# Kernel tuning notes

Measured on AMD Instinct MI355X. Metric: run time of the kernel, lower is better.

## Reference

```python
import jax, jax.numpy as jnp
import numpy as np

EPS = 1e-5

def wn(v, g):
    # weight_norm dim=0: each output row scaled to norm g
    return v * (g / jnp.linalg.norm(v, axis=1))[:, None]

def layernorm(h):
    mu = jnp.mean(h, axis=-1, keepdims=True)
    var = jnp.mean(jnp.square(h - mu), axis=-1, keepdims=True)
    return (h - mu) / jnp.sqrt(var + EPS)

def setup_inputs() -> dict:
    key = jax.random.key(0)
    ks = jax.random.split(key, 12)
    N, G = 200000, 256
    node_dim, cond_dim, out_dim = 256, 256, 512
    H = out_dim // 2  # 256
    s = lambda d: 1.0 / np.sqrt(d)
    return {
        "x": jax.random.normal(ks[0], (N, node_dim), jnp.float32),
        "cond": jax.random.normal(ks[1], (G, cond_dim), jnp.float32),
        "batch_ids": jax.random.randint(ks[2], (N,), 0, G, jnp.int32),
        # FiLM cond projection: Linear(cond_dim, 2H) weight-normed, with bias
        "v_cond": jax.random.normal(ks[3], (2 * H, cond_dim), jnp.float32) * s(cond_dim),
        "g_cond": jnp.ones((2 * H,), jnp.float32),
        "b_cond": jnp.zeros((2 * H,), jnp.float32),
        # FiLM main linear: Linear(node_dim, H) weight-normed, no bias
        "v1": jax.random.normal(ks[4], (H, node_dim), jnp.float32) * s(node_dim),
        "g1": jnp.ones((H,), jnp.float32),
        # head MLP: Linear(H,H)+ReLU+Linear(H,out_dim), both weight-normed, with bias
        "v2": jax.random.normal(ks[5], (H, H), jnp.float32) * s(H),
        "g2": jnp.ones((H,), jnp.float32),
        "b2": jnp.zeros((H,), jnp.float32),
        "v3": jax.random.normal(ks[6], (out_dim, H), jnp.float32) * s(H),
        "g3": jnp.ones((out_dim,), jnp.float32),
        "b3": jnp.zeros((out_dim,), jnp.float32),
    }

def reference(x, cond, batch_ids, v_cond, g_cond, b_cond, v1, g1, v2, g2, b2, v3, g3, b3):
    H = v1.shape[0]
    # per-graph FiLM params
    gb = cond @ wn(v_cond, g_cond).T + b_cond          # [G, 2H]
    gamma = gb[:, :H] + 1.0                            # [G, H]
    beta = gb[:, H:]                                   # [G, H]
    # node path: linear (no bias) + layernorm (no affine)
    h = layernorm(x @ wn(v1, g1).T)                    # [N, H]
    # gather per-graph FiLM to nodes, modulate, relu
    h = jax.nn.relu(h * gamma[batch_ids] + beta[batch_ids])
    # head MLP
    h = jax.nn.relu(h @ wn(v2, g2).T + b2)             # [N, H]
    logits = h @ wn(v3, g3).T + b3                     # [N, out_dim]
    return logits
```

## Files before the change

kernel.cpp:

```cpp
#include <hip/hip_runtime.h>

typedef __bf16 bf16x8 __attribute__((ext_vector_type(8)));
typedef float f32x16 __attribute__((ext_vector_type(16)));

#define K_DIM 256

__global__ void wn_kernel(const float* __restrict__ v, const float* __restrict__ gv,
                          __bf16* __restrict__ dstb, float* __restrict__ dstf) {
  const int r = blockIdx.x;
  const int l = threadIdx.x;
  const float* vr = v + (size_t)r * K_DIM;
  float4 p = *reinterpret_cast<const float4*>(vr + l * 4);
  float ss = p.x * p.x + p.y * p.y + p.z * p.z + p.w * p.w;
#pragma unroll
  for (int m = 1; m <= 32; m <<= 1) ss += __shfl_xor(ss, m, 64);
  const float sc = gv[r] * rsqrtf(ss);
  const float a0 = p.x * sc, a1 = p.y * sc, a2 = p.z * sc, a3 = p.w * sc;
  if (dstf != nullptr) {
    float4 o; o.x = a0; o.y = a1; o.z = a2; o.w = a3;
    *reinterpret_cast<float4*>(dstf + (size_t)r * K_DIM + l * 4) = o;
  }
  if (dstb != nullptr) {
    const int rows = gridDim.x;
    __bf16* d = dstb + ((size_t)(l >> 1) * rows + r) * 8 + (l & 1) * 4;
    d[0] = (__bf16)a0; d[1] = (__bf16)a1; d[2] = (__bf16)a2; d[3] = (__bf16)a3;
  }
}

__global__ void gb_kernel(const float* __restrict__ cond, const float* __restrict__ wncf,
                          const float* __restrict__ bc, float* __restrict__ gbuf) {
  const int gidx = blockIdx.x;
  const int t = threadIdx.x;
  __shared__ float c[256];
  c[t] = cond[(size_t)gidx * 256 + t];
  __syncthreads();
#pragma unroll
  for (int h = 0; h < 2; ++h) {
    const int o = (h << 8) + t;
    const float* wr = wncf + (size_t)o * 256;
    float s = 0.0f;
#pragma unroll 8
    for (int k = 0; k < 256; k += 4) {
      const float4 w4 = *reinterpret_cast<const float4*>(wr + k);
      s += c[k] * w4.x + c[k + 1] * w4.y + c[k + 2] * w4.z + c[k + 3] * w4.w;
    }
    gbuf[(size_t)gidx * 512 + o] = s + bc[o] + (h == 0 ? 1.0f : 0.0f);
  }
}

__global__ __launch_bounds__(128, 2) void fused_kernel(
    const float* __restrict__ x, const int* __restrict__ bids,
    const __bf16* __restrict__ W1t, const __bf16* __restrict__ W2t,
    const __bf16* __restrict__ W3t, const float* __restrict__ gbuf,
    const float* __restrict__ b2, const float* __restrict__ b3,
    float* __restrict__ out, const int n) {
  __shared__ __bf16 Abuf[32 * 64 * 8];
  __shared__ __bf16 Wbuf[4 * 256 * 8];

  const int t = threadIdx.x;
  const int lane = t & 63;
  const int wave = t >> 6;
  const int nlo = lane & 31;
  const int g = lane >> 5;
  const int mbase = wave << 5;
  const int R = blockIdx.x << 6;

  f32x16 zero;
#pragma unroll
  for (int e = 0; e < 16; ++e) zero[e] = 0.0f;

  f32x16 acc[8];

  auto stage_w = [&](const __bf16* wsrc, int kt, int outr, int outbase) {
#pragma unroll
    for (int it = 0; it < 8; ++it) {
      const int cid = (((wave << 3) + it) << 6) + lane;
      const int kc = cid >> 8;
      const int outl = cid & 255;
      const __bf16* gp = wsrc + ((size_t)((kt * 4 + kc) * outr + outbase + outl) << 3);
      __builtin_amdgcn_global_load_lds(
          (__attribute__((address_space(1))) void*)gp,
          (__attribute__((address_space(3))) void*)(&Wbuf[((wave << 3) + it) << 9]),
          16, 0, 0);
    }
  };

#pragma unroll
  for (int nt = 0; nt < 8; ++nt) acc[nt] = zero;
  {
    int row = R + mbase + nlo;
    if (row >= n) row = n - 1;
    const float* xrow = x + (size_t)row * K_DIM;
    for (int kt = 0; kt < 8; ++kt) {
      __syncthreads();
      stage_w(W1t, kt, 256, 0);
      __syncthreads();
#pragma unroll
      for (int ks = 0; ks < 2; ++ks) {
        const int k0 = kt * 32 + ks * 16 + g * 8;
        const float4 p = *reinterpret_cast<const float4*>(xrow + k0);
        const float4 q = *reinterpret_cast<const float4*>(xrow + k0 + 4);
        bf16x8 a;
        a[0] = (__bf16)p.x; a[1] = (__bf16)p.y; a[2] = (__bf16)p.z; a[3] = (__bf16)p.w;
        a[4] = (__bf16)q.x; a[5] = (__bf16)q.y; a[6] = (__bf16)q.z; a[7] = (__bf16)q.w;
#pragma unroll
        for (int nt = 0; nt < 8; ++nt) {
          const bf16x8 b = *reinterpret_cast<const bf16x8*>(
              &Wbuf[((((ks << 1) + g) << 8) + (nt << 5) + nlo) << 3]);
          acc[nt] = __builtin_amdgcn_mfma_f32_32x32x16_bf16(a, b, acc[nt], 0, 0, 0);
        }
      }
    }
  }

  {
    float mu[16], rs[16];
#pragma unroll
    for (int reg = 0; reg < 16; ++reg) {
      float s = 0.0f, q = 0.0f;
#pragma unroll
      for (int nt = 0; nt < 8; ++nt) {
        const float v = acc[nt][reg];
        s += v; q += v * v;
      }
#pragma unroll
      for (int m = 1; m <= 16; m <<= 1) {
        s += __shfl_xor(s, m, 64);
        q += __shfl_xor(q, m, 64);
      }
      const float mean = s * (1.0f / 256.0f);
      const float var = q * (1.0f / 256.0f) - mean * mean;
      mu[reg] = mean;
      rs[reg] = rsqrtf(var + 1e-5f);
    }
#pragma unroll
    for (int reg = 0; reg < 16; ++reg) {
      const int rl = (reg & 3) + ((reg >> 2) << 3) + (g << 2);
      int rglob = R + mbase + rl;
      if (rglob >= n) rglob = n - 1;
      const int bid = bids[rglob];
      const float* grow = gbuf + ((size_t)bid << 9);
#pragma unroll
      for (int nt = 0; nt < 8; ++nt) {
        const int col = (nt << 5) + nlo;
        float v = (acc[nt][reg] - mu[reg]) * rs[reg];
        v = v * grow[col] + grow[256 + col];
        v = v > 0.0f ? v : 0.0f;
        Abuf[((((col >> 3) << 6) + mbase + rl) << 3) + (col & 7)] = (__bf16)v;
      }
    }
  }

#pragma unroll
  for (int nt = 0; nt < 8; ++nt) acc[nt] = zero;
  for (int kt = 0; kt < 8; ++kt) {
    __syncthreads();
    stage_w(W2t, kt, 256, 0);
    __syncthreads();
#pragma unroll
    for (int ks = 0; ks < 2; ++ks) {
      const int kc = kt * 4 + ks * 2 + g;
      const bf16x8 a = *reinterpret_cast<const bf16x8*>(
          &Abuf[((kc << 6) + mbase + nlo) << 3]);
#pragma unroll
      for (int nt = 0; nt < 8; ++nt) {
        const bf16x8 b = *reinterpret_cast<const bf16x8*>(
            &Wbuf[((((ks << 1) + g) << 8) + (nt << 5) + nlo) << 3]);
        acc[nt] = __builtin_amdgcn_mfma_f32_32x32x16_bf16(a, b, acc[nt], 0, 0, 0);
      }
    }
  }
  {
    float b2v[8];
#pragma unroll
    for (int nt = 0; nt < 8; ++nt) b2v[nt] = b2[(nt << 5) + nlo];
#pragma unroll
    for (int reg = 0; reg < 16; ++reg) {
      const int rl = (reg & 3) + ((reg >> 2) << 3) + (g << 2);
#pragma unroll
      for (int nt = 0; nt < 8; ++nt) {
        const int col = (nt << 5) + nlo;
        float v = acc[nt][reg] + b2v[nt];
        v = v > 0.0f ? v : 0.0f;
        Abuf[((((col >> 3) << 6) + mbase + rl) << 3) + (col & 7)] = (__bf16)v;
      }
    }
  }

  for (int half = 0; half < 2; ++half) {
#pragma unroll
    for (int nt = 0; nt < 8; ++nt) acc[nt] = zero;
    for (int kt = 0; kt < 8; ++kt) {
      __syncthreads();
      stage_w(W3t, kt, 512, half << 8);
      __syncthreads();
#pragma unroll
      for (int ks = 0; ks < 2; ++ks) {
        const int kc = kt * 4 + ks * 2 + g;
        const bf16x8 a = *reinterpret_cast<const bf16x8*>(
            &Abuf[((kc << 6) + mbase + nlo) << 3]);
#pragma unroll
        for (int nt = 0; nt < 8; ++nt) {
          const bf16x8 b = *reinterpret_cast<const bf16x8*>(
              &Wbuf[((((ks << 1) + g) << 8) + (nt << 5) + nlo) << 3]);
          acc[nt] = __builtin_amdgcn_mfma_f32_32x32x16_bf16(a, b, acc[nt], 0, 0, 0);
        }
      }
    }
    float b3v[8];
#pragma unroll
    for (int nt = 0; nt < 8; ++nt) b3v[nt] = b3[(half << 8) + (nt << 5) + nlo];
#pragma unroll
    for (int reg = 0; reg < 16; ++reg) {
      const int rl = (reg & 3) + ((reg >> 2) << 3) + (g << 2);
      const int rglob = R + mbase + rl;
      if (rglob < n) {
        float* orow = out + (size_t)rglob * 512 + (half << 8);
#pragma unroll
        for (int nt = 0; nt < 8; ++nt) orow[(nt << 5) + nlo] = acc[nt][reg] + b3v[nt];
      }
    }
  }
}

extern "C" void kernel_launch(void* const* d_in, const int* in_sizes, int n_in,
                              void* d_out, int out_size, void* d_ws, size_t ws_size,
                              hipStream_t stream) {
  const float* x      = (const float*)d_in[0];
  const float* cond   = (const float*)d_in[1];
  const int*   bids   = (const int*)d_in[2];
  const float* v_cond = (const float*)d_in[3];
  const float* g_cond = (const float*)d_in[4];
  const float* b_cond = (const float*)d_in[5];
  const float* v1     = (const float*)d_in[6];
  const float* g1     = (const float*)d_in[7];
  const float* v2     = (const float*)d_in[8];
  const float* g2     = (const float*)d_in[9];
  const float* b2     = (const float*)d_in[10];
  const float* v3     = (const float*)d_in[11];
  const float* g3     = (const float*)d_in[12];
  const float* b3     = (const float*)d_in[13];
  float* out = (float*)d_out;
  const int n = in_sizes[0] / K_DIM;

  char* ws = (char*)d_ws;
  __bf16* W1t = (__bf16*)ws;
  __bf16* W2t = W1t + 65536;
  __bf16* W3t = W2t + 65536;
  float* wncf = (float*)(W3t + 131072);
  float* gbuf = wncf + 131072;

  wn_kernel<<<256, 64, 0, stream>>>(v1, g1, W1t, nullptr);
  wn_kernel<<<256, 64, 0, stream>>>(v2, g2, W2t, nullptr);
  wn_kernel<<<512, 64, 0, stream>>>(v3, g3, W3t, nullptr);
  wn_kernel<<<512, 64, 0, stream>>>(v_cond, g_cond, nullptr, wncf);
  gb_kernel<<<256, 256, 0, stream>>>(cond, wncf, b_cond, gbuf);

  const int nb = (n + 63) / 64;
  fused_kernel<<<nb, 128, 0, stream>>>(x, bids, W1t, W2t, W3t, gbuf, b2, b3, out, n);
}
```

Measured before the change: 722.2 us.

## Double rows per block, swizzle activation LDS, split W3 layout into halves

The fused MLP block grows from 64 to 128 rows with 4 waves, so each staged weight tile in LDS is reused by twice as many rows and each wave issues half as many staging loads. The activation buffer in LDS gets an XOR swizzle on the row index to reduce bank conflicts. The x loads for both k-substeps are issued before the barrier so they overlap the weight staging. W3 is laid out as two contiguous 256-output halves. Each block now uses twice the Abuf LDS and more threads, which may lower occupancy.

```diff
diff --git a/kernel.cpp b/kernel.cpp
--- a/kernel.cpp
+++ b/kernel.cpp
@@ -21,8 +21,8 @@
     *reinterpret_cast<float4*>(dstf + (size_t)r * K_DIM + l * 4) = o;
   }
   if (dstb != nullptr) {
-    const int rows = gridDim.x;
-    __bf16* d = dstb + ((size_t)(l >> 1) * rows + r) * 8 + (l & 1) * 4;
+    __bf16* d = dstb + ((size_t)(r >> 8) << 16) +
+                ((size_t)((l >> 1) << 8) + (r & 255)) * 8 + (l & 1) * 4;
     d[0] = (__bf16)a0; d[1] = (__bf16)a1; d[2] = (__bf16)a2; d[3] = (__bf16)a3;
   }
 }
@@ -48,22 +48,24 @@
   }
 }
 
-__global__ __launch_bounds__(128, 2) void fused_kernel(
+__global__ __launch_bounds__(256, 2) void fused_kernel(
     const float* __restrict__ x, const int* __restrict__ bids,
     const __bf16* __restrict__ W1t, const __bf16* __restrict__ W2t,
     const __bf16* __restrict__ W3t, const float* __restrict__ gbuf,
     const float* __restrict__ b2, const float* __restrict__ b3,
     float* __restrict__ out, const int n) {
-  __shared__ __bf16 Abuf[32 * 64 * 8];
+  __shared__ __bf16 Abuf[32 * 128 * 8];
   __shared__ __bf16 Wbuf[4 * 256 * 8];
 
   const int t = threadIdx.x;
   const int lane = t & 63;
-  const int wave = t >> 6;
+  const int w = t >> 6;
   const int nlo = lane & 31;
   const int g = lane >> 5;
-  const int mbase = wave << 5;
-  const int R = blockIdx.x << 6;
+  const int mbase = w << 5;
+  const int R = blockIdx.x << 7;
+
+  auto aidx = [](int kc, int row) { return ((kc << 7) + (row ^ (kc & 7))) << 3; };
 
   f32x16 zero;
 #pragma unroll
@@ -73,14 +75,14 @@
 
   auto stage_w = [&](const __bf16* wsrc, int kt, int outr, int outbase) {
 #pragma unroll
-    for (int it = 0; it < 8; ++it) {
-      const int cid = (((wave << 3) + it) << 6) + lane;
+    for (int it = 0; it < 4; ++it) {
+      const int cid = (((w << 2) + it) << 6) + lane;
       const int kc = cid >> 8;
       const int outl = cid & 255;
       const __bf16* gp = wsrc + ((size_t)((kt * 4 + kc) * outr + outbase + outl) << 3);
       __builtin_amdgcn_global_load_lds(
-          (__attribute__((address_space(1))) void*)gp,
-          (__attribute__((address_space(3))) void*)(&Wbuf[((wave << 3) + it) << 9]),
+          (const __attribute__((address_space(1))) void*)gp,
+          (__attribute__((address_space(3))) void*)(&Wbuf[(((w << 2) + it)) << 9]),
           16, 0, 0);
     }
   };
@@ -94,20 +96,24 @@
     for (int kt = 0; kt < 8; ++kt) {
       __syncthreads();
       stage_w(W1t, kt, 256, 0);
+      const int k0 = kt * 32 + g * 8;
+      const float4 p0 = *reinterpret_cast<const float4*>(xrow + k0);
+      const float4 q0 = *reinterpret_cast<const float4*>(xrow + k0 + 4);
+      const float4 p1 = *reinterpret_cast<const float4*>(xrow + k0 + 16);
+      const float4 q1 = *reinterpret_cast<const float4*>(xrow + k0 + 20);
+      bf16x8 a[2];
+      a[0][0] = (__bf16)p0.x; a[0][1] = (__bf16)p0.y; a[0][2] = (__bf16)p0.z; a[0][3] = (__bf16)p0.w;
+      a[0][4] = (__bf16)q0.x; a[0][5] = (__bf16)q0.y; a[0][6] = (__bf16)q0.z; a[0][7] = (__bf16)q0.w;
+      a[1][0] = (__bf16)p1.x; a[1][1] = (__bf16)p1.y; a[1][2] = (__bf16)p1.z; a[1][3] = (__bf16)p1.w;
+      a[1][4] = (__bf16)q1.x; a[1][5] = (__bf16)q1.y; a[1][6] = (__bf16)q1.z; a[1][7] = (__bf16)q1.w;
       __syncthreads();
 #pragma unroll
       for (int ks = 0; ks < 2; ++ks) {
-        const int k0 = kt * 32 + ks * 16 + g * 8;
-        const float4 p = *reinterpret_cast<const float4*>(xrow + k0);
-        const float4 q = *reinterpret_cast<const float4*>(xrow + k0 + 4);
-        bf16x8 a;
-        a[0] = (__bf16)p.x; a[1] = (__bf16)p.y; a[2] = (__bf16)p.z; a[3] = (__bf16)p.w;
-        a[4] = (__bf16)q.x; a[5] = (__bf16)q.y; a[6] = (__bf16)q.z; a[7] = (__bf16)q.w;
 #pragma unroll
         for (int nt = 0; nt < 8; ++nt) {
           const bf16x8 b = *reinterpret_cast<const bf16x8*>(
               &Wbuf[((((ks << 1) + g) << 8) + (nt << 5) + nlo) << 3]);
-          acc[nt] = __builtin_amdgcn_mfma_f32_32x32x16_bf16(a, b, acc[nt], 0, 0, 0);
+          acc[nt] = __builtin_amdgcn_mfma_f32_32x32x16_bf16(a[ks], b, acc[nt], 0, 0, 0);
         }
       }
     }
@@ -140,13 +146,14 @@
       if (rglob >= n) rglob = n - 1;
       const int bid = bids[rglob];
       const float* grow = gbuf + ((size_t)bid << 9);
+      const int rowi = mbase + rl;
 #pragma unroll
       for (int nt = 0; nt < 8; ++nt) {
         const int col = (nt << 5) + nlo;
         float v = (acc[nt][reg] - mu[reg]) * rs[reg];
         v = v * grow[col] + grow[256 + col];
         v = v > 0.0f ? v : 0.0f;
-        Abuf[((((col >> 3) << 6) + mbase + rl) << 3) + (col & 7)] = (__bf16)v;
+        Abuf[aidx(col >> 3, rowi) + (col & 7)] = (__bf16)v;
       }
     }
   }
@@ -159,9 +166,8 @@
     __syncthreads();
 #pragma unroll
     for (int ks = 0; ks < 2; ++ks) {
-      const int kc = kt * 4 + ks * 2 + g;
-      const bf16x8 a = *reinterpret_cast<const bf16x8*>(
-          &Abuf[((kc << 6) + mbase + nlo) << 3]);
+      const int kcf = kt * 4 + ks * 2 + g;
+      const bf16x8 a = *reinterpret_cast<const bf16x8*>(&Abuf[aidx(kcf, mbase + nlo)]);
 #pragma unroll
       for (int nt = 0; nt < 8; ++nt) {
         const bf16x8 b = *reinterpret_cast<const bf16x8*>(
@@ -177,12 +183,13 @@
 #pragma unroll
     for (int reg = 0; reg < 16; ++reg) {
       const int rl = (reg & 3) + ((reg >> 2) << 3) + (g << 2);
+      const int rowi = mbase + rl;
 #pragma unroll
       for (int nt = 0; nt < 8; ++nt) {
         const int col = (nt << 5) + nlo;
         float v = acc[nt][reg] + b2v[nt];
         v = v > 0.0f ? v : 0.0f;
-        Abuf[((((col >> 3) << 6) + mbase + rl) << 3) + (col & 7)] = (__bf16)v;
+        Abuf[aidx(col >> 3, rowi) + (col & 7)] = (__bf16)v;
       }
     }
   }
@@ -190,15 +197,15 @@
   for (int half = 0; half < 2; ++half) {
 #pragma unroll
     for (int nt = 0; nt < 8; ++nt) acc[nt] = zero;
+    const __bf16* w3h = W3t + ((size_t)half << 16);
     for (int kt = 0; kt < 8; ++kt) {
       __syncthreads();
-      stage_w(W3t, kt, 512, half << 8);
+      stage_w(w3h, kt, 256, 0);
       __syncthreads();
 #pragma unroll
       for (int ks = 0; ks < 2; ++ks) {
-        const int kc = kt * 4 + ks * 2 + g;
-        const bf16x8 a = *reinterpret_cast<const bf16x8*>(
-            &Abuf[((kc << 6) + mbase + nlo) << 3]);
+        const int kcf = kt * 4 + ks * 2 + g;
+        const bf16x8 a = *reinterpret_cast<const bf16x8*>(&Abuf[aidx(kcf, mbase + nlo)]);
 #pragma unroll
         for (int nt = 0; nt < 8; ++nt) {
           const bf16x8 b = *reinterpret_cast<const bf16x8*>(
@@ -256,6 +263,6 @@
   wn_kernel<<<512, 64, 0, stream>>>(v_cond, g_cond, nullptr, wncf);
   gb_kernel<<<256, 256, 0, stream>>>(cond, wncf, b_cond, gbuf);
 
-  const int nb = (n + 63) / 64;
-  fused_kernel<<<nb, 128, 0, stream>>>(x, bids, W1t, W2t, W3t, gbuf, b2, b3, out, n);
-}
+  const int nb = (n + 127) / 128;
+  fused_kernel<<<nb, 256, 0, stream>>>(x, bids, W1t, W2t, W3t, gbuf, b2, b3, out, n);
+}
```

Result: no change. 726.2 us (+0.6%).
